# Kernel tuning notes

Measured on AMD Instinct MI355X. Metric: run time of the kernel, lower is better.

The kernel has to match this reference:

```python
import jax, jax.numpy as jnp
import numpy as np

N_NODES = 100000

def gcn_conv(x, edge_index, W, b, n_nodes):
    # GCNConv: out = D^{-1/2} (A + I) D^{-1/2} X W + b  (self-loops added)
    src, dst = edge_index[0], edge_index[1]
    loops = jnp.arange(n_nodes, dtype=edge_index.dtype)
    src = jnp.concatenate([src, loops])
    dst = jnp.concatenate([dst, loops])
    deg = jax.ops.segment_sum(jnp.ones_like(dst, dtype=x.dtype), dst, num_segments=n_nodes)
    dinv = jnp.where(deg > 0, jax.lax.rsqrt(deg), 0.0)
    norm = dinv[src] * dinv[dst]  # [E+N]
    h = x @ W  # transform first (small d), then gather/scatter
    msgs = h[src] * norm[:, None]
    out = jax.ops.segment_sum(msgs, dst, num_segments=n_nodes)
    return out + b


def setup_inputs() -> dict:
    key = jax.random.key(0)
    k1, k2, k3, k4, k5, k6 = jax.random.split(key, 6)
    x = jax.random.normal(k1, (N_NODES, 3), dtype=jnp.float32)
    edge_index = jax.random.randint(k2, (2, 2400000), 0, N_NODES, dtype=jnp.int64)
    # Glorot-style init for GCNConv linear weights; zero bias matches PyG default
    W1 = jax.random.normal(k3, (3, 16), dtype=jnp.float32) * (1.0 / np.sqrt(3))
    b1 = jnp.zeros((16,), dtype=jnp.float32)
    W2 = jax.random.normal(k4, (16, 32), dtype=jnp.float32) * (1.0 / np.sqrt(16))
    b2 = jnp.zeros((32,), dtype=jnp.float32)
    return {"x": x, "edge_index": edge_index, "W1": W1, "b1": b1, "W2": W2, "b2": b2}


def reference(x, edge_index, W1, b1, W2, b2):
    n = x.shape[0]
    h = gcn_conv(x, edge_index, W1, b1, n)
    h = jax.nn.relu(h)
    h = gcn_conv(h, edge_index, W2, b2, n)
    # batch is all zeros in the original forward -> single-graph mean pool
    return jnp.mean(h, axis=0, keepdims=True)  # [1, 32]
```

## Files before the change

### kernel.cpp

```cpp
#include <hip/hip_runtime.h>

typedef unsigned int uint;
typedef unsigned long long ull;
typedef unsigned char uchar;


#define MAXB  256
#define CAP   16384u
#define BINB  512
#define CHUNK 4096
#define AFS   2048.0f
#define AFB   16384
#define AFM   0x1FFFFFu
#define PADN  131072

__global__ void __launch_bounds__(BINB)
bin2_kernel(const int* __restrict__ srcI, const int* __restrict__ dstI,
            uint* __restrict__ curDg, uint* __restrict__ curSg,
            uint* __restrict__ bufD, uint* __restrict__ bufS, int E) {
    __shared__ uint cntD[MAXB], scanD[MAXB], deltaD[MAXB];
    __shared__ uint cntS[MAXB], scanS[MAXB], deltaS[MAXB];
    __shared__ uint stageD[CHUNK];
    __shared__ uint stageS[CHUNK];
    __shared__ uchar stBD[CHUNK];
    __shared__ uchar stBS[CHUNK];
    const int tid = threadIdx.x;
    const int e0 = blockIdx.x * CHUNK;
    const int nE = min(CHUNK, E - e0);
    const int my0 = tid * 8;
    const int myc = max(0, min(8, nE - my0));
    if (tid < MAXB) cntD[tid] = 0u; else cntS[tid - MAXB] = 0u;

    uint d8[8], s8[8], rD[8], rS[8];
    if (myc == 8) {
        int4 ka = ((const int4*)(dstI + e0))[tid * 2];
        int4 kb = ((const int4*)(dstI + e0))[tid * 2 + 1];
        int4 oa = ((const int4*)(srcI + e0))[tid * 2];
        int4 ob = ((const int4*)(srcI + e0))[tid * 2 + 1];
        d8[0] = ka.x; d8[1] = ka.y; d8[2] = ka.z; d8[3] = ka.w;
        d8[4] = kb.x; d8[5] = kb.y; d8[6] = kb.z; d8[7] = kb.w;
        s8[0] = oa.x; s8[1] = oa.y; s8[2] = oa.z; s8[3] = oa.w;
        s8[4] = ob.x; s8[5] = ob.y; s8[6] = ob.z; s8[7] = ob.w;
    } else {
        for (int r = 0; r < myc; ++r) {
            d8[r] = (uint)dstI[e0 + my0 + r];
            s8[r] = (uint)srcI[e0 + my0 + r];
        }
    }
    __syncthreads();
    for (int r = 0; r < myc; ++r) {
        rD[r] = atomicAdd(&cntD[d8[r] >> 9], 1u);
        rS[r] = atomicAdd(&cntS[s8[r] >> 9], 1u);
    }
    __syncthreads();
    const int half = tid >> 8;
    const int li = tid & 255;
    uint* cn = half ? cntS : cntD;
    uint* sc = half ? scanS : scanD;
    sc[li] = cn[li];
    __syncthreads();
    for (int d = 1; d < MAXB; d <<= 1) {
        uint t = (li >= d) ? sc[li - d] : 0u;
        __syncthreads();
        sc[li] += t;
        __syncthreads();
    }
    {
        uint* cur = half ? curSg : curDg;
        uint* dl = half ? deltaS : deltaD;
        uint gbase = (uint)li * CAP + (cn[li] ? atomicAdd(&cur[li * 16], cn[li]) : 0u);
        dl[li] = gbase - (sc[li] - cn[li]);
    }
    __syncthreads();
    for (int r = 0; r < myc; ++r) {
        uint bD = d8[r] >> 9;
        uint pD = (scanD[bD] - cntD[bD]) + rD[r];
        stageD[pD] = ((d8[r] & 511u) << 17) | s8[r];
        stBD[pD] = (uchar)bD;
        uint bS = s8[r] >> 9;
        uint pS = (scanS[bS] - cntS[bS]) + rS[r];
        stageS[pS] = ((s8[r] & 511u) << 17) | d8[r];
        stBS[pS] = (uchar)bS;
    }
    __syncthreads();
#pragma unroll
    for (int r = 0; r < 8; ++r) {
        int i = r * BINB + tid;
        if (i < nE) {
            uint b = stBD[i];
            uint gp = deltaD[b] + (uint)i;
            if (gp < (b + 1u) * CAP) bufD[gp] = stageD[i];
            uint b2 = stBS[i];
            uint gp2 = deltaS[b2] + (uint)i;
            if (gp2 < (b2 + 1u) * CAP) bufS[gp2] = stageS[i];
        }
    }
}

__global__ void __launch_bounds__(1024)
degnode_kernel(const uint* __restrict__ buf, const uint* __restrict__ curD,
               const float* __restrict__ x, uint* __restrict__ degg,
               float* __restrict__ dinv, ull* __restrict__ pxd, int n) {
    __shared__ uint dg[512];
    const int tid = threadIdx.x;
    const int b = blockIdx.x;
    const uint base = (uint)b * CAP;
    const uint c = min(curD[b * 16], CAP);
    if (tid < 512) dg[tid] = 0u;
    __syncthreads();
    for (uint i0 = (uint)tid * 8u; i0 < c; i0 += 8192u) {
        uint cnt8 = min(8u, c - i0);
        uint en[8];
        if (cnt8 == 8u) {
            uint4 a = ((const uint4*)(buf + base + i0))[0];
            uint4 bb = ((const uint4*)(buf + base + i0))[1];
            en[0] = a.x; en[1] = a.y; en[2] = a.z; en[3] = a.w;
            en[4] = bb.x; en[5] = bb.y; en[6] = bb.z; en[7] = bb.w;
        } else {
            for (uint r = 0; r < cnt8; ++r) en[r] = buf[base + i0 + r];
        }
        for (uint r = 0; r < cnt8; ++r) atomicAdd(&dg[en[r] >> 17], 1u);
    }
    __syncthreads();
    if (tid < 512) {
        int node = (b << 9) + tid;
        if (node < n) {
            uint d = dg[tid];
            degg[node] = d;
            float di = rsqrtf((float)(d + 1u));
            dinv[node] = di;
            ull f0 = (ull)(uint)((int)rintf(x[3 * node] * di * AFS) + AFB);
            ull f1 = (ull)(uint)((int)rintf(x[3 * node + 1] * di * AFS) + AFB);
            ull f2 = (ull)(uint)((int)rintf(x[3 * node + 2] * di * AFS) + AFB);
            pxd[node] = f0 | (f1 << 21) | (f2 << 42);
        }
    }
}

__global__ void __launch_bounds__(1024)
aggqT_kernel(const uint* __restrict__ bufD, const uint* __restrict__ curD,
             const uint* __restrict__ bufS, const uint* __restrict__ curS,
             const uint* __restrict__ degg, const float* __restrict__ dinv,
             const ull* __restrict__ pxd, const float* __restrict__ x,
             const float* __restrict__ W1, const float* __restrict__ b1,
             const float* __restrict__ W2, const float* __restrict__ b2,
             float* __restrict__ T, uint* __restrict__ doneCtr,
             float* __restrict__ out, int n) {
    __shared__ ull acc[512];
    __shared__ float gl[512];
    __shared__ float taccs[16];
    __shared__ float tval[16];
    __shared__ int lastB;
    const int tid = threadIdx.x;
    const int b = blockIdx.x;
    const uint base = (uint)b * CAP;
    const uint cD = min(curD[b * 16], CAP);
    const uint cS = min(curS[b * 16], CAP);
    if (tid < 512) { acc[tid] = 0ull; gl[tid] = 0.0f; }
    if (tid < 16) taccs[tid] = 0.0f;
    __syncthreads();
    const int sweep = tid >> 9;
    const uint ht = (uint)(tid & 511);
    if (sweep == 0) {
        for (uint i0 = ht * 8u; i0 < cS; i0 += 4096u) {
            uint cnt8 = min(8u, cS - i0);
            uint en[8];
            if (cnt8 == 8u) {
                uint4 a = ((const uint4*)(bufS + base + i0))[0];
                uint4 bb = ((const uint4*)(bufS + base + i0))[1];
                en[0] = a.x; en[1] = a.y; en[2] = a.z; en[3] = a.w;
                en[4] = bb.x; en[5] = bb.y; en[6] = bb.z; en[7] = bb.w;
            } else {
                for (uint r = 0; r < cnt8; ++r) en[r] = bufS[base + i0 + r];
                for (uint r = cnt8; r < 8u; ++r) en[r] = en[0];
            }
            float dv[8];
#pragma unroll
            for (int r = 0; r < 8; ++r) dv[r] = dinv[en[r] & 0x1FFFFu];
#pragma unroll
            for (uint r = 0; r < 8u; ++r)
                if (r < cnt8) atomicAdd(&gl[en[r] >> 17], dv[r]);
        }
    } else {
        for (uint i0 = ht * 8u; i0 < cD; i0 += 4096u) {
            uint cnt8 = min(8u, cD - i0);
            uint en[8];
            if (cnt8 == 8u) {
                uint4 a = ((const uint4*)(bufD + base + i0))[0];
                uint4 bb = ((const uint4*)(bufD + base + i0))[1];
                en[0] = a.x; en[1] = a.y; en[2] = a.z; en[3] = a.w;
                en[4] = bb.x; en[5] = bb.y; en[6] = bb.z; en[7] = bb.w;
            } else {
                for (uint r = 0; r < cnt8; ++r) en[r] = bufD[base + i0 + r];
                for (uint r = cnt8; r < 8u; ++r) en[r] = en[0];
            }
            ull gv[8];
#pragma unroll
            for (int r = 0; r < 8; ++r) gv[r] = pxd[en[r] & 0x1FFFFu];
#pragma unroll
            for (uint r = 0; r < 8u; ++r)
                if (r < cnt8) atomicAdd(&acc[en[r] >> 17], gv[r]);
        }
    }
    __syncthreads();
    float sq[16];
#pragma unroll
    for (int k = 0; k < 16; ++k) sq[k] = 0.0f;
    if (tid < 512) {
        int node = (b << 9) + tid;
        if (node < n) {
            ull v = acc[tid];
            int ub = (int)(degg[node] * (uint)AFB);
            float di = dinv[node];
            const float isc = 1.0f / AFS;
            float av = (float)((int)(uint)(v & AFM) - ub) * isc + x[3 * node] * di;
            float bv = (float)((int)(uint)((v >> 21) & AFM) - ub) * isc + x[3 * node + 1] * di;
            float cv = (float)((int)(uint)((v >> 42) & AFM) - ub) * isc + x[3 * node + 2] * di;
            float w = gl[tid] + di;
#pragma unroll
            for (int k = 0; k < 16; ++k) {
                float h = di * (av * W1[k] + bv * W1[16 + k] + cv * W1[32 + k]) + b1[k];
                h = fmaxf(h, 0.0f);
                sq[k] = w * (di * h);
            }
        }
    }
#pragma unroll
    for (int k = 0; k < 16; ++k) {
        float v2 = sq[k];
        for (int off = 32; off > 0; off >>= 1) v2 += __shfl_down(v2, off, 64);
        if ((tid & 63) == 0) atomicAdd(&taccs[k], v2);
    }
    __syncthreads();
    if (tid < 16 && taccs[tid] != 0.0f) atomicAdd(&T[tid], taccs[tid]);
    __syncthreads();
    if (tid == 0) {
        __threadfence();
        uint t = atomicAdd(doneCtr, 1u);
        lastB = (t == (uint)(gridDim.x - 1)) ? 1 : 0;
    }
    __syncthreads();
    if (lastB) {
        if (tid < 16) tval[tid] = atomicAdd(&T[tid], 0.0f);
        __syncthreads();
        if (tid < 32) {
            float s2 = 0.0f;
#pragma unroll
            for (int k = 0; k < 16; ++k) s2 += tval[k] * W2[k * 32 + tid];
            out[tid] = b2[tid] + (1.0f / (float)n) * s2;
        }
    }
}

extern "C" void kernel_launch(void* const* d_in, const int* in_sizes, int n_in,
                              void* d_out, int out_size, void* d_ws, size_t ws_size,
                              hipStream_t stream) {
    const float* x   = (const float*)d_in[0];
    const int*   ei  = (const int*)d_in[1];
    const float* W1  = (const float*)d_in[2];
    const float* b1  = (const float*)d_in[3];
    const float* W2  = (const float*)d_in[4];
    const float* b2  = (const float*)d_in[5];
    float* out = (float*)d_out;

    const int n = in_sizes[0] / 3;
    const int E = in_sizes[1] / 2;
    const int* src = ei;
    const int* dst = ei + E;

    char* p = (char*)d_ws;
    float* T    = (float*)p;    p += 64;
    uint*  done = (uint*)p;     p += 64;
    uint*  curD = (uint*)p;     p += MAXB * 16 * 4;
    uint*  curS = (uint*)p;     p += MAXB * 16 * 4;
    size_t zbytes = (size_t)(p - (char*)d_ws);
    uint*  degg  = (uint*)p;    p += (size_t)n * 4;
    float* dinv  = (float*)p;   p += (size_t)n * 4;
    uint*  bufD  = (uint*)p;    p += (size_t)MAXB * CAP * 4;
    uint*  bufS  = (uint*)p;    p += (size_t)MAXB * CAP * 4;
    p = (char*)(((size_t)p + 31) & ~(size_t)31);
    ull*   pxd   = (ull*)p;     p += (size_t)PADN * 8;

    const int nb = (n + 511) >> 9;

    hipMemsetAsync(d_ws, 0, zbytes, stream);
    bin2_kernel<<<(E + CHUNK - 1) / CHUNK, BINB, 0, stream>>>(src, dst, curD, curS, bufD, bufS, E);
    degnode_kernel<<<nb, 1024, 0, stream>>>(bufD, curD, x, degg, dinv, pxd, n);
    aggqT_kernel<<<nb, 1024, 0, stream>>>(bufD, curD, bufS, curS, degg, dinv, pxd, x,
                                          W1, b1, W2, b2, T, done, out, n);
}
```

Measured before the change: 135.8 us.

## Fuse binning, degree and aggregation kernels into one persistent kernel with grid barriers

Replaces three kernel launches with a single persistent kernel of 256 blocks that pulls edge chunks through an atomic work-stealing counter, then crosses two software grid barriers for the degree and aggregation phases. The degree array is kept in shared memory instead of global memory. This removes launch gaps and tail effects between phases. In exchange it relies on all 256 blocks being co-resident for the spin barriers, and the binning stage now runs 1024-thread blocks that each handle 4 edges per thread.

```diff
diff --git a/kernel.cpp b/kernel.cpp
--- a/kernel.cpp
+++ b/kernel.cpp
@@ -7,182 +7,144 @@
 
 #define MAXB  256
 #define CAP   16384u
-#define BINB  512
+#define NTHR  1024
+#define NBLK  256
 #define CHUNK 4096
 #define AFS   2048.0f
 #define AFB   16384
 #define AFM   0x1FFFFFu
 #define PADN  131072
 
-__global__ void __launch_bounds__(BINB)
-bin2_kernel(const int* __restrict__ srcI, const int* __restrict__ dstI,
-            uint* __restrict__ curDg, uint* __restrict__ curSg,
-            uint* __restrict__ bufD, uint* __restrict__ bufS, int E) {
+__device__ __forceinline__ void gbar(uint* ctr, uint target) {
+    __syncthreads();
+    if (threadIdx.x == 0) {
+        __threadfence();
+        atomicAdd(ctr, 1u);
+        uint guard = 0u;
+        while (__hip_atomic_load(ctr, __ATOMIC_ACQUIRE,
+                                 __HIP_MEMORY_SCOPE_AGENT) < target) {
+            __builtin_amdgcn_s_sleep(8);
+            if (++guard > 0x20000000u) break;
+        }
+    }
+    __syncthreads();
+}
+
+__global__ void __launch_bounds__(NTHR, 4)
+mega(const int* __restrict__ srcI, const int* __restrict__ dstI,
+     const float* __restrict__ x,
+     const float* __restrict__ W1, const float* __restrict__ b1,
+     const float* __restrict__ W2, const float* __restrict__ b2,
+     uint* __restrict__ curDg, uint* __restrict__ curSg,
+     uint* __restrict__ bufD, uint* __restrict__ bufS,
+     float* __restrict__ dinv, ull* __restrict__ pxd,
+     float* __restrict__ T, uint* __restrict__ bar0, uint* __restrict__ bar1,
+     uint* __restrict__ wsteal, uint* __restrict__ doneCtr,
+     float* __restrict__ out, int n, int E, int nchunks) {
     __shared__ uint cntD[MAXB], scanD[MAXB], deltaD[MAXB];
     __shared__ uint cntS[MAXB], scanS[MAXB], deltaS[MAXB];
     __shared__ uint stageD[CHUNK];
     __shared__ uint stageS[CHUNK];
     __shared__ uchar stBD[CHUNK];
     __shared__ uchar stBS[CHUNK];
-    const int tid = threadIdx.x;
-    const int e0 = blockIdx.x * CHUNK;
-    const int nE = min(CHUNK, E - e0);
-    const int my0 = tid * 8;
-    const int myc = max(0, min(8, nE - my0));
-    if (tid < MAXB) cntD[tid] = 0u; else cntS[tid - MAXB] = 0u;
-
-    uint d8[8], s8[8], rD[8], rS[8];
-    if (myc == 8) {
-        int4 ka = ((const int4*)(dstI + e0))[tid * 2];
-        int4 kb = ((const int4*)(dstI + e0))[tid * 2 + 1];
-        int4 oa = ((const int4*)(srcI + e0))[tid * 2];
-        int4 ob = ((const int4*)(srcI + e0))[tid * 2 + 1];
-        d8[0] = ka.x; d8[1] = ka.y; d8[2] = ka.z; d8[3] = ka.w;
-        d8[4] = kb.x; d8[5] = kb.y; d8[6] = kb.z; d8[7] = kb.w;
-        s8[0] = oa.x; s8[1] = oa.y; s8[2] = oa.z; s8[3] = oa.w;
-        s8[4] = ob.x; s8[5] = ob.y; s8[6] = ob.z; s8[7] = ob.w;
-    } else {
-        for (int r = 0; r < myc; ++r) {
-            d8[r] = (uint)dstI[e0 + my0 + r];
-            s8[r] = (uint)srcI[e0 + my0 + r];
-        }
-    }
-    __syncthreads();
-    for (int r = 0; r < myc; ++r) {
-        rD[r] = atomicAdd(&cntD[d8[r] >> 9], 1u);
-        rS[r] = atomicAdd(&cntS[s8[r] >> 9], 1u);
-    }
-    __syncthreads();
-    const int half = tid >> 8;
-    const int li = tid & 255;
-    uint* cn = half ? cntS : cntD;
-    uint* sc = half ? scanS : scanD;
-    sc[li] = cn[li];
-    __syncthreads();
-    for (int d = 1; d < MAXB; d <<= 1) {
-        uint t = (li >= d) ? sc[li - d] : 0u;
-        __syncthreads();
-        sc[li] += t;
-        __syncthreads();
-    }
-    {
-        uint* cur = half ? curSg : curDg;
-        uint* dl = half ? deltaS : deltaD;
-        uint gbase = (uint)li * CAP + (cn[li] ? atomicAdd(&cur[li * 16], cn[li]) : 0u);
-        dl[li] = gbase - (sc[li] - cn[li]);
-    }
-    __syncthreads();
-    for (int r = 0; r < myc; ++r) {
-        uint bD = d8[r] >> 9;
-        uint pD = (scanD[bD] - cntD[bD]) + rD[r];
-        stageD[pD] = ((d8[r] & 511u) << 17) | s8[r];
-        stBD[pD] = (uchar)bD;
-        uint bS = s8[r] >> 9;
-        uint pS = (scanS[bS] - cntS[bS]) + rS[r];
-        stageS[pS] = ((s8[r] & 511u) << 17) | d8[r];
-        stBS[pS] = (uchar)bS;
-    }
-    __syncthreads();
-#pragma unroll
-    for (int r = 0; r < 8; ++r) {
-        int i = r * BINB + tid;
-        if (i < nE) {
-            uint b = stBD[i];
-            uint gp = deltaD[b] + (uint)i;
-            if (gp < (b + 1u) * CAP) bufD[gp] = stageD[i];
-            uint b2 = stBS[i];
-            uint gp2 = deltaS[b2] + (uint)i;
-            if (gp2 < (b2 + 1u) * CAP) bufS[gp2] = stageS[i];
-        }
-    }
-}
-
-__global__ void __launch_bounds__(1024)
-degnode_kernel(const uint* __restrict__ buf, const uint* __restrict__ curD,
-               const float* __restrict__ x, uint* __restrict__ degg,
-               float* __restrict__ dinv, ull* __restrict__ pxd, int n) {
     __shared__ uint dg[512];
+    __shared__ ull acc[512];
+    __shared__ float gl[512];
+    __shared__ float taccs[16], tval[16];
+    __shared__ int lastB;
+    __shared__ uint chsh;
     const int tid = threadIdx.x;
     const int b = blockIdx.x;
+    const int nb = (n + 511) >> 9;
+
+    for (;;) {
+        if (tid == 0) chsh = atomicAdd(wsteal, 1u);
+        __syncthreads();
+        const uint ch = chsh;
+        __syncthreads();
+        if (ch >= (uint)nchunks) break;
+        const int e0 = (int)ch * CHUNK;
+        const int nE = min(CHUNK, E - e0);
+        const int my0 = tid * 4;
+        const int myc = max(0, min(4, nE - my0));
+        if (tid < MAXB) { cntD[tid] = 0u; cntS[tid] = 0u; }
+
+        uint d4[4], s4[4], rD[4], rS[4];
+        if (myc == 4) {
+            int4 ka = ((const int4*)(dstI + e0))[tid];
+            int4 oa = ((const int4*)(srcI + e0))[tid];
+            d4[0] = ka.x; d4[1] = ka.y; d4[2] = ka.z; d4[3] = ka.w;
+            s4[0] = oa.x; s4[1] = oa.y; s4[2] = oa.z; s4[3] = oa.w;
+        } else {
+            for (int r = 0; r < myc; ++r) {
+                d4[r] = (uint)dstI[e0 + my0 + r];
+                s4[r] = (uint)srcI[e0 + my0 + r];
+            }
+        }
+        __syncthreads();
+        for (int r = 0; r < myc; ++r) {
+            rD[r] = atomicAdd(&cntD[d4[r] >> 9], 1u);
+            rS[r] = atomicAdd(&cntS[s4[r] >> 9], 1u);
+        }
+        __syncthreads();
+        const int half = tid >> 8;
+        const int li = tid & 255;
+        if (tid < 512) {
+            uint* cn = half ? cntS : cntD;
+            uint* sc = half ? scanS : scanD;
+            sc[li] = cn[li];
+        }
+        __syncthreads();
+        for (int d = 1; d < MAXB; d <<= 1) {
+            uint t = 0u;
+            if (tid < 512 && li >= d) t = (half ? scanS : scanD)[li - d];
+            __syncthreads();
+            if (tid < 512 && li >= d) (half ? scanS : scanD)[li] += t;
+            __syncthreads();
+        }
+        if (tid < 512) {
+            uint* cn = half ? cntS : cntD;
+            uint* sc = half ? scanS : scanD;
+            uint* cur = half ? curSg : curDg;
+            uint* dl = half ? deltaS : deltaD;
+            uint gbase = (uint)li * CAP + (cn[li] ? atomicAdd(&cur[li * 16], cn[li]) : 0u);
+            dl[li] = gbase - (sc[li] - cn[li]);
+        }
+        __syncthreads();
+        for (int r = 0; r < myc; ++r) {
+            uint bD = d4[r] >> 9;
+            uint pD = (scanD[bD] - cntD[bD]) + rD[r];
+            stageD[pD] = ((d4[r] & 511u) << 17) | s4[r];
+            stBD[pD] = (uchar)bD;
+            uint bS = s4[r] >> 9;
+            uint pS = (scanS[bS] - cntS[bS]) + rS[r];
+            stageS[pS] = ((s4[r] & 511u) << 17) | d4[r];
+            stBS[pS] = (uchar)bS;
+        }
+        __syncthreads();
+#pragma unroll
+        for (int r = 0; r < 4; ++r) {
+            int i = r * NTHR + tid;
+            if (i < nE) {
+                uint bb = stBD[i];
+                uint gp = deltaD[bb] + (uint)i;
+                if (gp < (bb + 1u) * CAP) bufD[gp] = stageD[i];
+                uint b2s = stBS[i];
+                uint gp2 = deltaS[b2s] + (uint)i;
+                if (gp2 < (b2s + 1u) * CAP) bufS[gp2] = stageS[i];
+            }
+        }
+        __syncthreads();
+    }
+    gbar(bar0, NBLK);
+
     const uint base = (uint)b * CAP;
-    const uint c = min(curD[b * 16], CAP);
-    if (tid < 512) dg[tid] = 0u;
-    __syncthreads();
-    for (uint i0 = (uint)tid * 8u; i0 < c; i0 += 8192u) {
-        uint cnt8 = min(8u, c - i0);
-        uint en[8];
-        if (cnt8 == 8u) {
-            uint4 a = ((const uint4*)(buf + base + i0))[0];
-            uint4 bb = ((const uint4*)(buf + base + i0))[1];
-            en[0] = a.x; en[1] = a.y; en[2] = a.z; en[3] = a.w;
-            en[4] = bb.x; en[5] = bb.y; en[6] = bb.z; en[7] = bb.w;
-        } else {
-            for (uint r = 0; r < cnt8; ++r) en[r] = buf[base + i0 + r];
-        }
-        for (uint r = 0; r < cnt8; ++r) atomicAdd(&dg[en[r] >> 17], 1u);
-    }
-    __syncthreads();
-    if (tid < 512) {
-        int node = (b << 9) + tid;
-        if (node < n) {
-            uint d = dg[tid];
-            degg[node] = d;
-            float di = rsqrtf((float)(d + 1u));
-            dinv[node] = di;
-            ull f0 = (ull)(uint)((int)rintf(x[3 * node] * di * AFS) + AFB);
-            ull f1 = (ull)(uint)((int)rintf(x[3 * node + 1] * di * AFS) + AFB);
-            ull f2 = (ull)(uint)((int)rintf(x[3 * node + 2] * di * AFS) + AFB);
-            pxd[node] = f0 | (f1 << 21) | (f2 << 42);
-        }
-    }
-}
-
-__global__ void __launch_bounds__(1024)
-aggqT_kernel(const uint* __restrict__ bufD, const uint* __restrict__ curD,
-             const uint* __restrict__ bufS, const uint* __restrict__ curS,
-             const uint* __restrict__ degg, const float* __restrict__ dinv,
-             const ull* __restrict__ pxd, const float* __restrict__ x,
-             const float* __restrict__ W1, const float* __restrict__ b1,
-             const float* __restrict__ W2, const float* __restrict__ b2,
-             float* __restrict__ T, uint* __restrict__ doneCtr,
-             float* __restrict__ out, int n) {
-    __shared__ ull acc[512];
-    __shared__ float gl[512];
-    __shared__ float taccs[16];
-    __shared__ float tval[16];
-    __shared__ int lastB;
-    const int tid = threadIdx.x;
-    const int b = blockIdx.x;
-    const uint base = (uint)b * CAP;
-    const uint cD = min(curD[b * 16], CAP);
-    const uint cS = min(curS[b * 16], CAP);
-    if (tid < 512) { acc[tid] = 0ull; gl[tid] = 0.0f; }
-    if (tid < 16) taccs[tid] = 0.0f;
-    __syncthreads();
-    const int sweep = tid >> 9;
-    const uint ht = (uint)(tid & 511);
-    if (sweep == 0) {
-        for (uint i0 = ht * 8u; i0 < cS; i0 += 4096u) {
-            uint cnt8 = min(8u, cS - i0);
-            uint en[8];
-            if (cnt8 == 8u) {
-                uint4 a = ((const uint4*)(bufS + base + i0))[0];
-                uint4 bb = ((const uint4*)(bufS + base + i0))[1];
-                en[0] = a.x; en[1] = a.y; en[2] = a.z; en[3] = a.w;
-                en[4] = bb.x; en[5] = bb.y; en[6] = bb.z; en[7] = bb.w;
-            } else {
-                for (uint r = 0; r < cnt8; ++r) en[r] = bufS[base + i0 + r];
-                for (uint r = cnt8; r < 8u; ++r) en[r] = en[0];
-            }
-            float dv[8];
-#pragma unroll
-            for (int r = 0; r < 8; ++r) dv[r] = dinv[en[r] & 0x1FFFFu];
-#pragma unroll
-            for (uint r = 0; r < 8u; ++r)
-                if (r < cnt8) atomicAdd(&gl[en[r] >> 17], dv[r]);
-        }
-    } else {
-        for (uint i0 = ht * 8u; i0 < cD; i0 += 4096u) {
+    uint cD = 0u;
+    if (b < nb) {
+        cD = min(curDg[b * 16], CAP);
+        if (tid < 512) dg[tid] = 0u;
+        __syncthreads();
+        for (uint i0 = (uint)tid * 8u; i0 < cD; i0 += 8192u) {
             uint cnt8 = min(8u, cD - i0);
             uint en[8];
             if (cnt8 == 8u) {
@@ -192,39 +154,99 @@
                 en[4] = bb.x; en[5] = bb.y; en[6] = bb.z; en[7] = bb.w;
             } else {
                 for (uint r = 0; r < cnt8; ++r) en[r] = bufD[base + i0 + r];
-                for (uint r = cnt8; r < 8u; ++r) en[r] = en[0];
-            }
-            ull gv[8];
-#pragma unroll
-            for (int r = 0; r < 8; ++r) gv[r] = pxd[en[r] & 0x1FFFFu];
-#pragma unroll
-            for (uint r = 0; r < 8u; ++r)
-                if (r < cnt8) atomicAdd(&acc[en[r] >> 17], gv[r]);
-        }
-    }
-    __syncthreads();
+            }
+            for (uint r = 0; r < cnt8; ++r) atomicAdd(&dg[en[r] >> 17], 1u);
+        }
+        __syncthreads();
+        if (tid < 512) {
+            int node = (b << 9) + tid;
+            if (node < n) {
+                float di = rsqrtf((float)(dg[tid] + 1u));
+                dinv[node] = di;
+                ull f0 = (ull)(uint)((int)rintf(x[3 * node] * di * AFS) + AFB);
+                ull f1 = (ull)(uint)((int)rintf(x[3 * node + 1] * di * AFS) + AFB);
+                ull f2 = (ull)(uint)((int)rintf(x[3 * node + 2] * di * AFS) + AFB);
+                pxd[node] = f0 | (f1 << 21) | (f2 << 42);
+            }
+        }
+    }
+    gbar(bar1, NBLK);
+
     float sq[16];
 #pragma unroll
     for (int k = 0; k < 16; ++k) sq[k] = 0.0f;
-    if (tid < 512) {
-        int node = (b << 9) + tid;
-        if (node < n) {
-            ull v = acc[tid];
-            int ub = (int)(degg[node] * (uint)AFB);
-            float di = dinv[node];
-            const float isc = 1.0f / AFS;
-            float av = (float)((int)(uint)(v & AFM) - ub) * isc + x[3 * node] * di;
-            float bv = (float)((int)(uint)((v >> 21) & AFM) - ub) * isc + x[3 * node + 1] * di;
-            float cv = (float)((int)(uint)((v >> 42) & AFM) - ub) * isc + x[3 * node + 2] * di;
-            float w = gl[tid] + di;
-#pragma unroll
-            for (int k = 0; k < 16; ++k) {
-                float h = di * (av * W1[k] + bv * W1[16 + k] + cv * W1[32 + k]) + b1[k];
-                h = fmaxf(h, 0.0f);
-                sq[k] = w * (di * h);
-            }
-        }
-    }
+    if (tid < 16) taccs[tid] = 0.0f;
+    if (b < nb) {
+        const uint cS = min(curSg[b * 16], CAP);
+        if (tid < 512) { acc[tid] = 0ull; gl[tid] = 0.0f; }
+        __syncthreads();
+        const int sweep = tid >> 9;
+        const uint ht = (uint)(tid & 511);
+        if (sweep == 0) {
+            for (uint i0 = ht * 8u; i0 < cS; i0 += 4096u) {
+                uint cnt8 = min(8u, cS - i0);
+                uint en[8];
+                if (cnt8 == 8u) {
+                    uint4 a = ((const uint4*)(bufS + base + i0))[0];
+                    uint4 bb = ((const uint4*)(bufS + base + i0))[1];
+                    en[0] = a.x; en[1] = a.y; en[2] = a.z; en[3] = a.w;
+                    en[4] = bb.x; en[5] = bb.y; en[6] = bb.z; en[7] = bb.w;
+                } else {
+                    for (uint r = 0; r < cnt8; ++r) en[r] = bufS[base + i0 + r];
+                    for (uint r = cnt8; r < 8u; ++r) en[r] = en[0];
+                }
+                float dv[8];
+#pragma unroll
+                for (int r = 0; r < 8; ++r) dv[r] = dinv[en[r] & 0x1FFFFu];
+#pragma unroll
+                for (uint r = 0; r < 8u; ++r)
+                    if (r < cnt8) atomicAdd(&gl[en[r] >> 17], dv[r]);
+            }
+        } else {
+            for (uint i0 = ht * 8u; i0 < cD; i0 += 4096u) {
+                uint cnt8 = min(8u, cD - i0);
+                uint en[8];
+                if (cnt8 == 8u) {
+                    uint4 a = ((const uint4*)(bufD + base + i0))[0];
+                    uint4 bb = ((const uint4*)(bufD + base + i0))[1];
+                    en[0] = a.x; en[1] = a.y; en[2] = a.z; en[3] = a.w;
+                    en[4] = bb.x; en[5] = bb.y; en[6] = bb.z; en[7] = bb.w;
+                } else {
+                    for (uint r = 0; r < cnt8; ++r) en[r] = bufD[base + i0 + r];
+                    for (uint r = cnt8; r < 8u; ++r) en[r] = en[0];
+                }
+                ull gv[8];
+#pragma unroll
+                for (int r = 0; r < 8; ++r) gv[r] = pxd[en[r] & 0x1FFFFu];
+#pragma unroll
+                for (uint r = 0; r < 8u; ++r)
+                    if (r < cnt8) atomicAdd(&acc[en[r] >> 17], gv[r]);
+            }
+        }
+        __syncthreads();
+        if (tid < 512) {
+            int node = (b << 9) + tid;
+            if (node < n) {
+                ull v = acc[tid];
+                int ub = (int)(dg[tid] * (uint)AFB);
+                float di = rsqrtf((float)(dg[tid] + 1u));
+                const float isc = 1.0f / AFS;
+                float av = (float)((int)(uint)(v & AFM) - ub) * isc + x[3 * node] * di;
+                float bv = (float)((int)(uint)((v >> 21) & AFM) - ub) * isc + x[3 * node + 1] * di;
+                float cv = (float)((int)(uint)((v >> 42) & AFM) - ub) * isc + x[3 * node + 2] * di;
+                float w = gl[tid] + di;
+#pragma unroll
+                for (int k = 0; k < 16; ++k) {
+                    float h = di * (av * W1[k] + bv * W1[16 + k] + cv * W1[32 + k]) + b1[k];
+                    h = fmaxf(h, 0.0f);
+                    sq[k] = w * (di * h);
+                }
+            }
+        }
+    } else {
+        __syncthreads();
+    }
+    __syncthreads();
 #pragma unroll
     for (int k = 0; k < 16; ++k) {
         float v2 = sq[k];
@@ -237,7 +259,7 @@
     if (tid == 0) {
         __threadfence();
         uint t = atomicAdd(doneCtr, 1u);
-        lastB = (t == (uint)(gridDim.x - 1)) ? 1 : 0;
+        lastB = (t == (uint)(NBLK - 1)) ? 1 : 0;
     }
     __syncthreads();
     if (lastB) {
@@ -269,23 +291,25 @@
     const int* dst = ei + E;
 
     char* p = (char*)d_ws;
-    float* T    = (float*)p;    p += 64;
-    uint*  done = (uint*)p;     p += 64;
-    uint*  curD = (uint*)p;     p += MAXB * 16 * 4;
-    uint*  curS = (uint*)p;     p += MAXB * 16 * 4;
+    float* T     = (float*)p;   p += 64;
+    uint*  done  = (uint*)p;    p += 64;
+    uint*  bar0  = (uint*)p;    p += 64;
+    uint*  bar1  = (uint*)p;    p += 64;
+    uint*  wst   = (uint*)p;    p += 64;
+    uint*  curD  = (uint*)p;    p += MAXB * 16 * 4;
+    uint*  curS  = (uint*)p;    p += MAXB * 16 * 4;
     size_t zbytes = (size_t)(p - (char*)d_ws);
-    uint*  degg  = (uint*)p;    p += (size_t)n * 4;
     float* dinv  = (float*)p;   p += (size_t)n * 4;
     uint*  bufD  = (uint*)p;    p += (size_t)MAXB * CAP * 4;
     uint*  bufS  = (uint*)p;    p += (size_t)MAXB * CAP * 4;
     p = (char*)(((size_t)p + 31) & ~(size_t)31);
     ull*   pxd   = (ull*)p;     p += (size_t)PADN * 8;
 
-    const int nb = (n + 511) >> 9;
+    const int nchunks = (E + CHUNK - 1) / CHUNK;
 
     hipMemsetAsync(d_ws, 0, zbytes, stream);
-    bin2_kernel<<<(E + CHUNK - 1) / CHUNK, BINB, 0, stream>>>(src, dst, curD, curS, bufD, bufS, E);
-    degnode_kernel<<<nb, 1024, 0, stream>>>(bufD, curD, x, degg, dinv, pxd, n);
-    aggqT_kernel<<<nb, 1024, 0, stream>>>(bufD, curD, bufS, curS, degg, dinv, pxd, x,
-                                          W1, b1, W2, b2, T, done, out, n);
+    mega<<<NBLK, NTHR, 0, stream>>>(src, dst, x, W1, b1, W2, b2,
+                                    curD, curS, bufD, bufS, dinv, pxd,
+                                    T, bar0, bar1, wst, done, out,
+                                    n, E, nchunks);
 }
```

After: 186.0 us. 37.0% more time.
